# Kernel tuning notes

Hardware: AMD Instinct MI355X
Metric: run time of the kernel (lower is better)

Reference implementation:

```python
import jax, jax.numpy as jnp
import numpy as np

H, DH, D, S, B = 8, 64, 512, 512, 2
EPS = 1e-5

def _trop_linear(x, W):
    # y[..., o] = max_i (x[..., i] + W[o, i])
    return jnp.max(x[..., None, :] + W, axis=-1)

def _layer_norm(x, gamma, beta):
    mu = jnp.mean(x, axis=-1, keepdims=True)
    var = jnp.mean((x - mu) ** 2, axis=-1, keepdims=True)
    return (x - mu) * jax.lax.rsqrt(var + EPS) * gamma + beta

def setup_inputs() -> dict:
    key = jax.random.key(0)
    ks = jax.random.split(key, 8)
    sc = lambda fan_in: 1.0 / np.sqrt(fan_in)
    return {
        "h":   jax.random.normal(ks[0], (S, B, D), jnp.float32),
        "Wq":  jax.random.normal(ks[1], (H * DH, D), jnp.float32) * sc(D),
        "Wkv": jax.random.normal(ks[2], (2 * H * DH, D), jnp.float32) * sc(D),
        "Wqt": jax.random.normal(ks[3], (DH, DH), jnp.float32),
        "Wkt": jax.random.normal(ks[4], (DH, DH), jnp.float32),
        "Wvt": jax.random.normal(ks[5], (DH, DH), jnp.float32),
        "lam": jnp.ones((1, 1, D), jnp.float32),
        "Wo":  jax.random.normal(ks[6], (D, H * DH), jnp.float32) * sc(H * DH),
        "gamma": jnp.ones((D,), jnp.float32),
        "beta":  jnp.zeros((D,), jnp.float32),
    }

def reference(h, Wq, Wkv, Wqt, Wkt, Wvt, lam, Wo, gamma, beta):
    # h: [S, B, D]; mems=None so c == h; pre_lnorm=False
    c = h
    head_q = h @ Wq.T                                # [S, B, H*DH]
    kv = c @ Wkv.T                                   # [S, B, 2*H*DH]
    head_k, head_v = jnp.split(kv, 2, axis=-1)

    norm = lambda x: jnp.log1p(jax.nn.relu(x)) - lam  # tropical normalize
    head_q, head_k, head_v = norm(head_q), norm(head_k), norm(head_v)

    # [S,B,H,DH] -> [B,S,H,DH] -> flat reshape to [B*H, S, DH] (matches torch)
    to_bh = lambda x: jnp.transpose(x.reshape(S, B, H, DH), (1, 0, 2, 3)).reshape(B * H, S, DH)
    q = _trop_linear(to_bh(head_q), Wqt)
    k = _trop_linear(to_bh(head_k), Wkt)
    v = _trop_linear(to_bh(head_v), Wvt)

    # tropical distance score: -(max_d(q-k) - min_d(q-k)) over head dim
    diff = q[:, :, None, :] - k[:, None, :, :]        # [BH, Sq, Sk, DH]
    attn_scores = -(jnp.max(diff, axis=-1) - jnp.min(diff, axis=-1))  # [BH,Sq,Sk]

    # max-plus aggregation: context = max_sk(score + v)
    sum_sv = attn_scores[..., None] + v[:, None, :, :]  # [BH, Sq, Sk, DH]
    context = jnp.max(sum_sv, axis=2)                   # [BH, Sq, DH]

    # flat reshape back (matches torch), permute, expm1
    context = context.reshape(B, H, S, DH)
    context = jnp.transpose(context, (2, 0, 1, 3))      # [S, B, H, DH]
    context = jnp.expm1(context)
    attn_vec = context.reshape(S, B, H * DH)

    attn_out = attn_vec @ Wo.T                          # [S, B, D]
    return _layer_norm(h + attn_out, gamma, beta)
```

## Files before the change

kernel.cpp:

```cpp
#include <hip/hip_runtime.h>
#include <cmath>

typedef __attribute__((ext_vector_type(8))) __bf16 bf16x8;
typedef __attribute__((ext_vector_type(4))) float f32x4;

namespace {
constexpr int GP = 512;
constexpr int WS_Q = 0;
constexpr int WS_K = 524288;
constexpr int WS_V = 1048576;
}

__device__ inline unsigned short f2bf(float x) {
  union { float f; unsigned u; } v; v.f = x;
  unsigned r = v.u + 0x7fff + ((v.u >> 16) & 1);
  return (unsigned short)(r >> 16);
}

__global__ __launch_bounds__(256) void k_conv(const float* __restrict__ h,
    const float* __restrict__ Wq, const float* __restrict__ Wkv,
    const float* __restrict__ Wo, unsigned short* __restrict__ hb,
    unsigned short* __restrict__ Wcb, unsigned short* __restrict__ Wob)
{
  int i = (blockIdx.x * 256 + threadIdx.x) * 4;
  float4 v; unsigned short* dst;
  if (i < 524288)        { v = *(const float4*)&h[i];             dst = hb  + i; }
  else if (i < 786432)   { v = *(const float4*)&Wq[i - 524288];   dst = Wcb + (i - 524288); }
  else if (i < 1310720)  { v = *(const float4*)&Wkv[i - 786432];  dst = Wcb + (i - 524288); }
  else                   { v = *(const float4*)&Wo[i - 1310720];  dst = Wob + (i - 1310720); }
  ushort4 o;
  o.x = f2bf(v.x); o.y = f2bf(v.y); o.z = f2bf(v.z); o.w = f2bf(v.w);
  *(ushort4*)dst = o;
}

template<int EPI>
__global__ __launch_bounds__(256) void k_gemm(const unsigned short* __restrict__ Ab,
    const unsigned short* __restrict__ Bb, const float* __restrict__ lam,
    float* __restrict__ outp)
{
  __shared__ unsigned short As[64][72];
  __shared__ unsigned short Bs[64][72];
  const int tid = threadIdx.x;
  const int r0 = blockIdx.y * 64, c0 = blockIdx.x * 64;
  const int w = tid >> 6, l = tid & 63;
  const int wr = (w >> 1) * 32, wc = (w & 1) * 32;
  const int srow = tid >> 3, sk8 = (tid & 7) * 8;
  f32x4 acc[2][2] = {};
  for (int kk = 0; kk < 512; kk += 64) {
    __syncthreads();
    *(int4*)&As[srow][sk8]      = *(const int4*)&Ab[(r0 + srow) * 512 + kk + sk8];
    *(int4*)&As[srow + 32][sk8] = *(const int4*)&Ab[(r0 + srow + 32) * 512 + kk + sk8];
    *(int4*)&Bs[srow][sk8]      = *(const int4*)&Bb[(c0 + srow) * 512 + kk + sk8];
    *(int4*)&Bs[srow + 32][sk8] = *(const int4*)&Bb[(c0 + srow + 32) * 512 + kk + sk8];
    __syncthreads();
    #pragma unroll
    for (int ks = 0; ks < 2; ++ks) {
      const int kc = ks * 32 + (l >> 4) * 8;
      bf16x8 a0 = *(const bf16x8*)&As[wr +      (l & 15)][kc];
      bf16x8 a1 = *(const bf16x8*)&As[wr + 16 + (l & 15)][kc];
      bf16x8 b0 = *(const bf16x8*)&Bs[wc +      (l & 15)][kc];
      bf16x8 b1 = *(const bf16x8*)&Bs[wc + 16 + (l & 15)][kc];
      acc[0][0] = __builtin_amdgcn_mfma_f32_16x16x32_bf16(a0, b0, acc[0][0], 0, 0, 0);
      acc[0][1] = __builtin_amdgcn_mfma_f32_16x16x32_bf16(a0, b1, acc[0][1], 0, 0, 0);
      acc[1][0] = __builtin_amdgcn_mfma_f32_16x16x32_bf16(a1, b0, acc[1][0], 0, 0, 0);
      acc[1][1] = __builtin_amdgcn_mfma_f32_16x16x32_bf16(a1, b1, acc[1][1], 0, 0, 0);
    }
  }
  #pragma unroll
  for (int i = 0; i < 2; ++i) {
    #pragma unroll
    for (int j = 0; j < 2; ++j) {
      #pragma unroll
      for (int r = 0; r < 4; ++r) {
        int row = r0 + wr + i * 16 + (l >> 4) * 4 + r;
        int col = c0 + wc + j * 16 + (l & 15);
        float x = acc[i][j][r];
        if constexpr (EPI == 0) {
          float val = log1pf(fmaxf(x, 0.f)) - lam[col & 511];
          int which = col >> 9, jq = col & 511;
          int hh = jq >> 6, di = jq & 63;
          int s = row >> 1, bb = row & 1;
          int gg = bb * 8 + (s >> 6);
          int pp = ((s & 63) << 3) | hh;
          outp[which * 524288 + ((gg << 9) + pp) * 64 + di] = val;
        } else {
          outp[row * 512 + col] = x;
        }
      }
    }
  }
}

__global__ __launch_bounds__(256) void k_trop(const float* __restrict__ nbuf,
    const float* __restrict__ Wqt, const float* __restrict__ Wkt,
    const float* __restrict__ Wvt, float* __restrict__ qkv)
{
  const int t = blockIdx.y;
  const float* Wt = (t == 0) ? Wqt : (t == 1) ? Wkt : Wvt;
  const float* in = nbuf + t * 524288;
  float* out = qkv + t * 524288;
  __shared__ float Wl[64][65];
  __shared__ float nl[64][64];
  const int tid = threadIdx.x;
  const int w = tid >> 6, lane = tid & 63;
  #pragma unroll
  for (int q = 0; q < 16; ++q) {
    int idx = q * 256 + tid;
    Wl[idx >> 6][idx & 63] = Wt[idx];
  }
  #pragma unroll
  for (int q = 0; q < 4; ++q) {
    int idx = q * 256 + tid;
    int row = idx >> 4, c4 = idx & 15;
    *(f32x4*)&nl[row][c4 * 4] =
        *(const f32x4*)&in[(blockIdx.x * 64 + row) * 64 + c4 * 4];
  }
  __syncthreads();
  float wreg[64];
  #pragma unroll
  for (int i = 0; i < 64; ++i) wreg[i] = Wl[lane][i];
  #pragma unroll 2
  for (int it = 0; it < 16; ++it) {
    int lrow = w * 16 + it;
    float m0 = -INFINITY, m1 = -INFINITY, m2 = -INFINITY, m3 = -INFINITY;
    #pragma unroll
    for (int i = 0; i < 64; i += 4) {
      f32x4 nv = *(const f32x4*)&nl[lrow][i];
      m0 = fmaxf(m0, nv[0] + wreg[i]);
      m1 = fmaxf(m1, nv[1] + wreg[i + 1]);
      m2 = fmaxf(m2, nv[2] + wreg[i + 2]);
      m3 = fmaxf(m3, nv[3] + wreg[i + 3]);
    }
    out[(blockIdx.x * 64 + lrow) * 64 + lane] = fmaxf(fmaxf(m0, m1), fmaxf(m2, m3));
  }
}

__global__ __launch_bounds__(256) void k_attn(const float* __restrict__ qkv,
    float* __restrict__ ctxp)
{
  const int pt = blockIdx.x;
  const int g  = blockIdx.y;
  const int cs = blockIdx.z;
  const float* qb = qkv + WS_Q + g * GP * 64;
  const float* kb = qkv + WS_K + g * GP * 64;
  const float* vb = qkv + WS_V + g * GP * 64;
  __shared__ float qs[32][64];
  __shared__ float ks[64][64];
  __shared__ float vs[64][64];
  __shared__ float ss[32][68];
  const int tid = threadIdx.x;
  const int tr = tid >> 4, tc = tid & 15;
  const int xb = tc & 7;
  #pragma unroll
  for (int q2 = 0; q2 < 2; ++q2) {
    int row = tr + q2 * 16;
    f32x4 v4 = *(const f32x4*)&qb[(pt * 32 + row) * 64 + tc * 4];
    *(f32x4*)&qs[row][((tc ^ (row & 7))) * 4] = v4;
  }
  float ctx[2][4];
  #pragma unroll
  for (int i = 0; i < 2; ++i)
    #pragma unroll
    for (int j = 0; j < 4; ++j) ctx[i][j] = -INFINITY;

  for (int cc = 0; cc < 2; ++cc) {
    const int c0 = cs * 128 + cc * 64;
    __syncthreads();
    #pragma unroll
    for (int q4 = 0; q4 < 4; ++q4) {
      int row = tr + q4 * 16;
      int sb = (tc ^ (row & 7)) * 4;
      *(f32x4*)&ks[row][sb] = *(const f32x4*)&kb[(c0 + row) * 64 + tc * 4];
      *(f32x4*)&vs[row][sb] = *(const f32x4*)&vb[(c0 + row) * 64 + tc * 4];
    }
    __syncthreads();
    float mx[2][4], mn[2][4];
    #pragma unroll
    for (int i = 0; i < 2; ++i)
      #pragma unroll
      for (int m = 0; m < 4; ++m) { mx[i][m] = -INFINITY; mn[i][m] = INFINITY; }
    const int r0 = tr * 2, r1 = r0 + 1;
    #pragma unroll 2
    for (int b = 0; b < 16; ++b) {
      f32x4 q0 = *(const f32x4*)&qs[r0][(b ^ (r0 & 7)) * 4];
      f32x4 q1 = *(const f32x4*)&qs[r1][(b ^ (r1 & 7)) * 4];
      const int kblk = (b ^ xb) * 4;
      #pragma unroll
      for (int m = 0; m < 4; ++m) {
        f32x4 kv = *(const f32x4*)&ks[tc + m * 16][kblk];
        #pragma unroll
        for (int e = 0; e < 4; ++e) {
          float d0 = q0[e] - kv[e];
          float d1 = q1[e] - kv[e];
          mx[0][m] = fmaxf(mx[0][m], d0); mn[0][m] = fminf(mn[0][m], d0);
          mx[1][m] = fmaxf(mx[1][m], d1); mn[1][m] = fminf(mn[1][m], d1);
        }
      }
    }
    #pragma unroll
    for (int i = 0; i < 2; ++i)
      #pragma unroll
      for (int m = 0; m < 4; ++m)
        ss[tr * 2 + i][tc + m * 16] = mn[i][m] - mx[i][m];
    __syncthreads();
    #pragma unroll 2
    for (int cb = 0; cb < 16; ++cb) {
      f32x4 s0 = *(const f32x4*)&ss[r0][cb * 4];
      f32x4 s1 = *(const f32x4*)&ss[r1][cb * 4];
      #pragma unroll
      for (int e = 0; e < 4; ++e) {
        int c = cb * 4 + e;
        f32x4 vv = *(const f32x4*)&vs[c][(tc ^ (c & 7)) * 4];
        #pragma unroll
        for (int j = 0; j < 4; ++j) {
          ctx[0][j] = fmaxf(ctx[0][j], s0[e] + vv[j]);
          ctx[1][j] = fmaxf(ctx[1][j], s1[e] + vv[j]);
        }
      }
    }
  }
  int base = cs * 524288 + g * 32768 + (pt * 32 + tr * 2) * 64 + tc * 4;
  f32x4 o0, o1;
  #pragma unroll
  for (int j = 0; j < 4; ++j) { o0[j] = ctx[0][j]; o1[j] = ctx[1][j]; }
  *(f32x4*)&ctxp[base]      = o0;
  *(f32x4*)&ctxp[base + 64] = o1;
}

__global__ __launch_bounds__(256) void k_comb(const float* __restrict__ ctxp,
    unsigned short* __restrict__ avb)
{
  int idx = blockIdx.x * 256 + threadIdx.x;
  int dblk = idx & 15, p = (idx >> 4) & 511, g = idx >> 13;
  const float* cp = ctxp + g * 32768 + p * 64 + dblk * 4;
  f32x4 a = *(const f32x4*)cp;
  f32x4 b = *(const f32x4*)(cp + 524288);
  f32x4 c = *(const f32x4*)(cp + 1048576);
  f32x4 d = *(const f32x4*)(cp + 1572864);
  ushort4 o;
  float v0 = fmaxf(fmaxf(a[0], b[0]), fmaxf(c[0], d[0]));
  float v1 = fmaxf(fmaxf(a[1], b[1]), fmaxf(c[1], d[1]));
  float v2 = fmaxf(fmaxf(a[2], b[2]), fmaxf(c[2], d[2]));
  float v3 = fmaxf(fmaxf(a[3], b[3]), fmaxf(c[3], d[3]));
  o.x = f2bf(expm1f(v0)); o.y = f2bf(expm1f(v1));
  o.z = f2bf(expm1f(v2)); o.w = f2bf(expm1f(v3));
  *(ushort4*)&avb[(p * 2 + (g >> 3)) * 512 + (g & 7) * 64 + dblk * 4] = o;
}

__global__ __launch_bounds__(256) void k_ln(const float* __restrict__ hin,
    const float* __restrict__ ao, const float* __restrict__ gamma,
    const float* __restrict__ beta, float* __restrict__ outp)
{
  const int r = blockIdx.x;
  const int tid = threadIdx.x;
  float2 hv = *(const float2*)&hin[r * 512 + tid * 2];
  float2 a2 = *(const float2*)&ao[r * 512 + tid * 2];
  float x0 = hv.x + a2.x, x1 = hv.y + a2.y;
  float sum = x0 + x1;
  float sq = x0 * x0 + x1 * x1;
  #pragma unroll
  for (int o = 32; o > 0; o >>= 1) {
    sum += __shfl_down(sum, o);
    sq  += __shfl_down(sq, o);
  }
  __shared__ float rs[8];
  const int lane = tid & 63, w = tid >> 6;
  if (lane == 0) { rs[w] = sum; rs[4 + w] = sq; }
  __syncthreads();
  float tot   = rs[0] + rs[1] + rs[2] + rs[3];
  float totsq = rs[4] + rs[5] + rs[6] + rs[7];
  float mu  = tot * (1.f / 512.f);
  float var = totsq * (1.f / 512.f) - mu * mu;
  float rstd = rsqrtf(fmaxf(var, 0.f) + 1e-5f);
  int c0 = tid * 2;
  outp[r * 512 + c0]     = (x0 - mu) * rstd * gamma[c0]     + beta[c0];
  outp[r * 512 + c0 + 1] = (x1 - mu) * rstd * gamma[c0 + 1] + beta[c0 + 1];
}

extern "C" void kernel_launch(void* const* d_in, const int* in_sizes, int n_in,
                              void* d_out, int out_size, void* d_ws, size_t ws_size,
                              hipStream_t stream) {
  const float* hin   = (const float*)d_in[0];
  const float* Wq    = (const float*)d_in[1];
  const float* Wkv   = (const float*)d_in[2];
  const float* Wqt   = (const float*)d_in[3];
  const float* Wkt   = (const float*)d_in[4];
  const float* Wvt   = (const float*)d_in[5];
  const float* lam   = (const float*)d_in[6];
  const float* Wo    = (const float*)d_in[7];
  const float* gamma = (const float*)d_in[8];
  const float* beta  = (const float*)d_in[9];
  char* wsb = (char*)d_ws;
  float*          qkvbuf = (float*)wsb;
  float*          nbuf   = (float*)(wsb + 6291456);
  float*          ctxp   = (float*)(wsb + 6291456);
  float*          ao     = (float*)(wsb + 6291456);
  unsigned short* avb    = (unsigned short*)wsb;
  unsigned short* hb     = (unsigned short*)(wsb + 12582912);
  unsigned short* Wcb    = (unsigned short*)(wsb + 13631488);
  unsigned short* Wob    = (unsigned short*)(wsb + 15204352);
  float* out = (float*)d_out;

  k_conv   <<<dim3(1536),       256, 0, stream>>>(hin, Wq, Wkv, Wo, hb, Wcb, Wob);
  k_gemm<0><<<dim3(24, 16),     256, 0, stream>>>(hb, Wcb, lam, nbuf);
  k_trop   <<<dim3(128, 3),     256, 0, stream>>>(nbuf, Wqt, Wkt, Wvt, qkvbuf);
  k_attn   <<<dim3(16, 16, 4),  256, 0, stream>>>(qkvbuf, ctxp);
  k_comb   <<<dim3(512),        256, 0, stream>>>(ctxp, avb);
  k_gemm<1><<<dim3(8, 16),      256, 0, stream>>>(avb, Wob, nullptr, ao);
  k_ln     <<<dim3(1024),       256, 0, stream>>>(hin, ao, gamma, beta, out);
}
```

Before: 83.29 us.

## Fuse bf16 conversion, tropical projection and context combine into GEMM kernels

Removes the standalone fp32-to-bf16 conversion kernel by converting h and weights on the fly while staging into shared memory. Fuses the per-head tropical linear into the QKV GEMM epilogue through a shared-memory tile, and fuses the split-context max-reduce plus expm1 into the A-operand load of the output GEMM. This cuts the launch count from seven to four and drops intermediate global round-trips. In exchange, each GEMM block now reads fp32 and repeats the conversion work, and the second GEMM redoes the combine and expm1 for every column tile.

```diff
diff --git a/kernel.cpp b/kernel.cpp
--- a/kernel.cpp
+++ b/kernel.cpp
@@ -17,41 +17,50 @@
   return (unsigned short)(r >> 16);
 }
 
-__global__ __launch_bounds__(256) void k_conv(const float* __restrict__ h,
+__device__ inline void cvt8_store(unsigned short* dst, float4 a, float4 b) {
+  ushort4 lo, hi;
+  lo.x = f2bf(a.x); lo.y = f2bf(a.y); lo.z = f2bf(a.z); lo.w = f2bf(a.w);
+  hi.x = f2bf(b.x); hi.y = f2bf(b.y); hi.z = f2bf(b.z); hi.w = f2bf(b.w);
+  *(ushort4*)dst = lo; *(ushort4*)(dst + 4) = hi;
+}
+
+__global__ __launch_bounds__(256) void k_gemm0t(const float* __restrict__ h,
     const float* __restrict__ Wq, const float* __restrict__ Wkv,
-    const float* __restrict__ Wo, unsigned short* __restrict__ hb,
-    unsigned short* __restrict__ Wcb, unsigned short* __restrict__ Wob)
-{
-  int i = (blockIdx.x * 256 + threadIdx.x) * 4;
-  float4 v; unsigned short* dst;
-  if (i < 524288)        { v = *(const float4*)&h[i];             dst = hb  + i; }
-  else if (i < 786432)   { v = *(const float4*)&Wq[i - 524288];   dst = Wcb + (i - 524288); }
-  else if (i < 1310720)  { v = *(const float4*)&Wkv[i - 786432];  dst = Wcb + (i - 524288); }
-  else                   { v = *(const float4*)&Wo[i - 1310720];  dst = Wob + (i - 1310720); }
-  ushort4 o;
-  o.x = f2bf(v.x); o.y = f2bf(v.y); o.z = f2bf(v.z); o.w = f2bf(v.w);
-  *(ushort4*)dst = o;
-}
-
-template<int EPI>
-__global__ __launch_bounds__(256) void k_gemm(const unsigned short* __restrict__ Ab,
-    const unsigned short* __restrict__ Bb, const float* __restrict__ lam,
-    float* __restrict__ outp)
+    const float* __restrict__ lam, const float* __restrict__ Wqt,
+    const float* __restrict__ Wkt, const float* __restrict__ Wvt,
+    float* __restrict__ qkv)
 {
   __shared__ unsigned short As[64][72];
   __shared__ unsigned short Bs[64][72];
+  __shared__ float Wl[64][65];
+  __shared__ float nl[64][68];
   const int tid = threadIdx.x;
-  const int r0 = blockIdx.y * 64, c0 = blockIdx.x * 64;
+  const int bx = blockIdx.x;
+  const int r0 = blockIdx.y * 64, c0 = bx * 64;
+  const int which = c0 >> 9;
+  const int hh = bx & 7;
+  const float* Wt = (which == 0) ? Wqt : (which == 1) ? Wkt : Wvt;
+  #pragma unroll
+  for (int q = 0; q < 16; ++q) {
+    int idx = q * 256 + tid;
+    Wl[idx >> 6][idx & 63] = Wt[idx];
+  }
   const int w = tid >> 6, l = tid & 63;
   const int wr = (w >> 1) * 32, wc = (w & 1) * 32;
   const int srow = tid >> 3, sk8 = (tid & 7) * 8;
   f32x4 acc[2][2] = {};
   for (int kk = 0; kk < 512; kk += 64) {
     __syncthreads();
-    *(int4*)&As[srow][sk8]      = *(const int4*)&Ab[(r0 + srow) * 512 + kk + sk8];
-    *(int4*)&As[srow + 32][sk8] = *(const int4*)&Ab[(r0 + srow + 32) * 512 + kk + sk8];
-    *(int4*)&Bs[srow][sk8]      = *(const int4*)&Bb[(c0 + srow) * 512 + kk + sk8];
-    *(int4*)&Bs[srow + 32][sk8] = *(const int4*)&Bb[(c0 + srow + 32) * 512 + kk + sk8];
+    #pragma unroll
+    for (int q2 = 0; q2 < 2; ++q2) {
+      int row = srow + q2 * 32;
+      const float* ap = &h[(r0 + row) * 512 + kk + sk8];
+      cvt8_store(&As[row][sk8], *(const float4*)ap, *(const float4*)(ap + 4));
+      int c = c0 + row;
+      const float* wrp = (c < 512) ? (Wq + c * 512) : (Wkv + (c - 512) * 512);
+      cvt8_store(&Bs[row][sk8], *(const float4*)&wrp[kk + sk8],
+                 *(const float4*)&wrp[kk + sk8 + 4]);
+    }
     __syncthreads();
     #pragma unroll
     for (int ks = 0; ks < 2; ++ks) {
@@ -67,71 +76,37 @@
     }
   }
   #pragma unroll
-  for (int i = 0; i < 2; ++i) {
-    #pragma unroll
-    for (int j = 0; j < 2; ++j) {
+  for (int i = 0; i < 2; ++i)
+    #pragma unroll
+    for (int j = 0; j < 2; ++j)
       #pragma unroll
       for (int r = 0; r < 4; ++r) {
-        int row = r0 + wr + i * 16 + (l >> 4) * 4 + r;
-        int col = c0 + wc + j * 16 + (l & 15);
-        float x = acc[i][j][r];
-        if constexpr (EPI == 0) {
-          float val = log1pf(fmaxf(x, 0.f)) - lam[col & 511];
-          int which = col >> 9, jq = col & 511;
-          int hh = jq >> 6, di = jq & 63;
-          int s = row >> 1, bb = row & 1;
-          int gg = bb * 8 + (s >> 6);
-          int pp = ((s & 63) << 3) | hh;
-          outp[which * 524288 + ((gg << 9) + pp) * 64 + di] = val;
-        } else {
-          outp[row * 512 + col] = x;
-        }
-      }
-    }
-  }
-}
-
-__global__ __launch_bounds__(256) void k_trop(const float* __restrict__ nbuf,
-    const float* __restrict__ Wqt, const float* __restrict__ Wkt,
-    const float* __restrict__ Wvt, float* __restrict__ qkv)
-{
-  const int t = blockIdx.y;
-  const float* Wt = (t == 0) ? Wqt : (t == 1) ? Wkt : Wvt;
-  const float* in = nbuf + t * 524288;
-  float* out = qkv + t * 524288;
-  __shared__ float Wl[64][65];
-  __shared__ float nl[64][64];
-  const int tid = threadIdx.x;
-  const int w = tid >> 6, lane = tid & 63;
-  #pragma unroll
-  for (int q = 0; q < 16; ++q) {
-    int idx = q * 256 + tid;
-    Wl[idx >> 6][idx & 63] = Wt[idx];
-  }
-  #pragma unroll
-  for (int q = 0; q < 4; ++q) {
-    int idx = q * 256 + tid;
-    int row = idx >> 4, c4 = idx & 15;
-    *(f32x4*)&nl[row][c4 * 4] =
-        *(const f32x4*)&in[(blockIdx.x * 64 + row) * 64 + c4 * 4];
-  }
+        int rl = wr + i * 16 + (l >> 4) * 4 + r;
+        int cl = wc + j * 16 + (l & 15);
+        nl[rl][cl] = log1pf(fmaxf(acc[i][j][r], 0.f)) - lam[hh * 64 + cl];
+      }
   __syncthreads();
   float wreg[64];
   #pragma unroll
-  for (int i = 0; i < 64; ++i) wreg[i] = Wl[lane][i];
+  for (int i = 0; i < 64; ++i) wreg[i] = Wl[l][i];
   #pragma unroll 2
   for (int it = 0; it < 16; ++it) {
-    int lrow = w * 16 + it;
+    int lr = w + it * 4;
     float m0 = -INFINITY, m1 = -INFINITY, m2 = -INFINITY, m3 = -INFINITY;
     #pragma unroll
     for (int i = 0; i < 64; i += 4) {
-      f32x4 nv = *(const f32x4*)&nl[lrow][i];
+      f32x4 nv = *(const f32x4*)&nl[lr][i];
       m0 = fmaxf(m0, nv[0] + wreg[i]);
       m1 = fmaxf(m1, nv[1] + wreg[i + 1]);
       m2 = fmaxf(m2, nv[2] + wreg[i + 2]);
       m3 = fmaxf(m3, nv[3] + wreg[i + 3]);
     }
-    out[(blockIdx.x * 64 + lrow) * 64 + lane] = fmaxf(fmaxf(m0, m1), fmaxf(m2, m3));
+    int r = r0 + lr;
+    int s = r >> 1, bb = r & 1;
+    int g = bb * 8 + (s >> 6);
+    int p = ((s & 63) << 3) | hh;
+    qkv[which * 524288 + ((g << 9) + p) * 64 + l] =
+        fmaxf(fmaxf(m0, m1), fmaxf(m2, m3));
   }
 }
 
@@ -227,24 +202,73 @@
   *(f32x4*)&ctxp[base + 64] = o1;
 }
 
-__global__ __launch_bounds__(256) void k_comb(const float* __restrict__ ctxp,
-    unsigned short* __restrict__ avb)
+__global__ __launch_bounds__(256) void k_gemm1c(const float* __restrict__ ctxp,
+    const float* __restrict__ Wo, float* __restrict__ ao)
 {
-  int idx = blockIdx.x * 256 + threadIdx.x;
-  int dblk = idx & 15, p = (idx >> 4) & 511, g = idx >> 13;
-  const float* cp = ctxp + g * 32768 + p * 64 + dblk * 4;
-  f32x4 a = *(const f32x4*)cp;
-  f32x4 b = *(const f32x4*)(cp + 524288);
-  f32x4 c = *(const f32x4*)(cp + 1048576);
-  f32x4 d = *(const f32x4*)(cp + 1572864);
-  ushort4 o;
-  float v0 = fmaxf(fmaxf(a[0], b[0]), fmaxf(c[0], d[0]));
-  float v1 = fmaxf(fmaxf(a[1], b[1]), fmaxf(c[1], d[1]));
-  float v2 = fmaxf(fmaxf(a[2], b[2]), fmaxf(c[2], d[2]));
-  float v3 = fmaxf(fmaxf(a[3], b[3]), fmaxf(c[3], d[3]));
-  o.x = f2bf(expm1f(v0)); o.y = f2bf(expm1f(v1));
-  o.z = f2bf(expm1f(v2)); o.w = f2bf(expm1f(v3));
-  *(ushort4*)&avb[(p * 2 + (g >> 3)) * 512 + (g & 7) * 64 + dblk * 4] = o;
+  __shared__ unsigned short As[64][72];
+  __shared__ unsigned short Bs[64][72];
+  const int tid = threadIdx.x;
+  const int r0 = blockIdx.y * 64, c0 = blockIdx.x * 64;
+  const int w = tid >> 6, l = tid & 63;
+  const int wr = (w >> 1) * 32, wc = (w & 1) * 32;
+  const int srow = tid >> 3, sk8 = (tid & 7) * 8;
+  f32x4 acc[2][2] = {};
+  for (int kk = 0; kk < 512; kk += 64) {
+    __syncthreads();
+    #pragma unroll
+    for (int q2 = 0; q2 < 2; ++q2) {
+      int row = srow + q2 * 32;
+      int r = r0 + row;
+      int p = r >> 1, b2 = r & 1;
+      int j0 = kk + sk8;
+      int h2 = j0 >> 6, d0 = j0 & 63;
+      const float* cp = ctxp + (b2 * 8 + h2) * 32768 + p * 64 + d0;
+      f32x4 m0 = *(const f32x4*)cp;
+      f32x4 m1 = *(const f32x4*)(cp + 4);
+      #pragma unroll
+      for (int cs = 1; cs < 4; ++cs) {
+        f32x4 a0 = *(const f32x4*)(cp + cs * 524288);
+        f32x4 a1 = *(const f32x4*)(cp + cs * 524288 + 4);
+        #pragma unroll
+        for (int e = 0; e < 4; ++e) {
+          m0[e] = fmaxf(m0[e], a0[e]);
+          m1[e] = fmaxf(m1[e], a1[e]);
+        }
+      }
+      ushort4 lo, hi;
+      lo.x = f2bf(expm1f(m0[0])); lo.y = f2bf(expm1f(m0[1]));
+      lo.z = f2bf(expm1f(m0[2])); lo.w = f2bf(expm1f(m0[3]));
+      hi.x = f2bf(expm1f(m1[0])); hi.y = f2bf(expm1f(m1[1]));
+      hi.z = f2bf(expm1f(m1[2])); hi.w = f2bf(expm1f(m1[3]));
+      *(ushort4*)&As[row][sk8] = lo;
+      *(ushort4*)&As[row][sk8 + 4] = hi;
+      const float* bp = &Wo[(c0 + row) * 512 + kk + sk8];
+      cvt8_store(&Bs[row][sk8], *(const float4*)bp, *(const float4*)(bp + 4));
+    }
+    __syncthreads();
+    #pragma unroll
+    for (int ks = 0; ks < 2; ++ks) {
+      const int kc = ks * 32 + (l >> 4) * 8;
+      bf16x8 a0 = *(const bf16x8*)&As[wr +      (l & 15)][kc];
+      bf16x8 a1 = *(const bf16x8*)&As[wr + 16 + (l & 15)][kc];
+      bf16x8 b0 = *(const bf16x8*)&Bs[wc +      (l & 15)][kc];
+      bf16x8 b1 = *(const bf16x8*)&Bs[wc + 16 + (l & 15)][kc];
+      acc[0][0] = __builtin_amdgcn_mfma_f32_16x16x32_bf16(a0, b0, acc[0][0], 0, 0, 0);
+      acc[0][1] = __builtin_amdgcn_mfma_f32_16x16x32_bf16(a0, b1, acc[0][1], 0, 0, 0);
+      acc[1][0] = __builtin_amdgcn_mfma_f32_16x16x32_bf16(a1, b0, acc[1][0], 0, 0, 0);
+      acc[1][1] = __builtin_amdgcn_mfma_f32_16x16x32_bf16(a1, b1, acc[1][1], 0, 0, 0);
+    }
+  }
+  #pragma unroll
+  for (int i = 0; i < 2; ++i)
+    #pragma unroll
+    for (int j = 0; j < 2; ++j)
+      #pragma unroll
+      for (int r = 0; r < 4; ++r) {
+        int row = r0 + wr + i * 16 + (l >> 4) * 4 + r;
+        int col = c0 + wc + j * 16 + (l & 15);
+        ao[row * 512 + col] = acc[i][j][r];
+      }
 }
 
 __global__ __launch_bounds__(256) void k_ln(const float* __restrict__ hin,
@@ -291,21 +315,13 @@
   const float* gamma = (const float*)d_in[8];
   const float* beta  = (const float*)d_in[9];
   char* wsb = (char*)d_ws;
-  float*          qkvbuf = (float*)wsb;
-  float*          nbuf   = (float*)(wsb + 6291456);
-  float*          ctxp   = (float*)(wsb + 6291456);
-  float*          ao     = (float*)(wsb + 6291456);
-  unsigned short* avb    = (unsigned short*)wsb;
-  unsigned short* hb     = (unsigned short*)(wsb + 12582912);
-  unsigned short* Wcb    = (unsigned short*)(wsb + 13631488);
-  unsigned short* Wob    = (unsigned short*)(wsb + 15204352);
-  float* out = (float*)d_out;
-
-  k_conv   <<<dim3(1536),       256, 0, stream>>>(hin, Wq, Wkv, Wo, hb, Wcb, Wob);
-  k_gemm<0><<<dim3(24, 16),     256, 0, stream>>>(hb, Wcb, lam, nbuf);
-  k_trop   <<<dim3(128, 3),     256, 0, stream>>>(nbuf, Wqt, Wkt, Wvt, qkvbuf);
-  k_attn   <<<dim3(16, 16, 4),  256, 0, stream>>>(qkvbuf, ctxp);
-  k_comb   <<<dim3(512),        256, 0, stream>>>(ctxp, avb);
-  k_gemm<1><<<dim3(8, 16),      256, 0, stream>>>(avb, Wob, nullptr, ao);
-  k_ln     <<<dim3(1024),       256, 0, stream>>>(hin, ao, gamma, beta, out);
-}
+  float* qkvbuf = (float*)wsb;
+  float* ctxp   = (float*)(wsb + 6291456);
+  float* ao     = (float*)wsb;
+  float* out    = (float*)d_out;
+
+  k_gemm0t<<<dim3(24, 16),    256, 0, stream>>>(hin, Wq, Wkv, lam, Wqt, Wkt, Wvt, qkvbuf);
+  k_attn  <<<dim3(16, 16, 4), 256, 0, stream>>>(qkvbuf, ctxp);
+  k_gemm1c<<<dim3(8, 16),     256, 0, stream>>>(ctxp, Wo, ao);
+  k_ln    <<<dim3(1024),      256, 0, stream>>>(hin, ao, gamma, beta, out);
+}
```

New measurement: 83.86 us. No clear change (+0.7%).
